# Optimization experiments

Measured on AMD Instinct MI355X. Metric: run time of the kernel, lower is better.

## Reference

```python
import jax, jax.numpy as jnp
import numpy as np


def setup_inputs() -> dict:
    key = jax.random.key(0)
    k1, k2, k3 = jax.random.split(key, 3)
    N, L, S, H, D = 2, 2048, 2048, 8, 64
    return {
        "queries": jax.random.normal(k1, (N, L, H, D), dtype=jnp.float32),
        "keys": jax.random.normal(k2, (N, S, H, D), dtype=jnp.float32),
        "values": jax.random.normal(k3, (N, S, H, D), dtype=jnp.float32),
        "q_mask": jnp.ones((N, L), dtype=bool),
        "kv_mask": jnp.ones((N, S), dtype=bool),
    }


def reference(queries, keys, values, q_mask, kv_mask):
    # QK^T: [N, L, S, H]
    qk = jnp.einsum("nlhd,nshd->nlsh", queries, keys)
    # mask: True where attention is allowed
    mask = q_mask[:, :, None, None] & kv_mask[:, None, :, None]
    qk = jnp.where(mask, qk, -jnp.inf)
    softmax_temp = 1.0 / np.sqrt(queries.shape[3]).astype(np.float32)
    A = jax.nn.softmax(softmax_temp * qk, axis=2)  # over S
    out = jnp.einsum("nlsh,nshd->nlhd", A, values)
    return out
```

## Files before the change

### kernel.cpp

```cpp
#include <hip/hip_runtime.h>
#include <hip/hip_bf16.h>

#define N_B 2
#define L_Q 2048
#define S_K 2048
#define N_H 8
#define D_H 64
#define HD  512
#define KVB 64
#define NT  32
#define RS  72
#define PQT ((size_t)N_B * L_Q * N_H)
#define LOG2E 1.4426950408889634f

typedef __attribute__((ext_vector_type(8))) short bf16x8;
typedef __attribute__((ext_vector_type(4))) short short4v;
typedef __attribute__((ext_vector_type(4))) float f32x4;

__device__ __forceinline__ short f2bf(float f) {
  union { float f; unsigned u; } v; v.f = f;
  return (short)((v.u + 0x7FFFu + ((v.u >> 16) & 1u)) >> 16);
}
__device__ __forceinline__ float bf2f(short s) {
  union { unsigned u; float f; } w; w.u = ((unsigned)(unsigned short)s) << 16;
  return w.f;
}
__device__ __forceinline__ bf16x8 pack8(float4 a, float4 b) {
  bf16x8 t;
  t[0]=f2bf(a.x); t[1]=f2bf(a.y); t[2]=f2bf(a.z); t[3]=f2bf(a.w);
  t[4]=f2bf(b.x); t[5]=f2bf(b.y); t[6]=f2bf(b.z); t[7]=f2bf(b.w);
  return t;
}

__global__ __launch_bounds__(256)
void preconv_kernel(const float* __restrict__ K, const float* __restrict__ V,
                    const int* __restrict__ kvm,
                    short* __restrict__ kws, short* __restrict__ vws,
                    unsigned long long* __restrict__ mws) {
  const size_t i = (size_t)blockIdx.x * 256 + threadIdx.x;
  const float4* kp = (const float4*)K + i * 2;
  float4 a = kp[0], b = kp[1];
  *(bf16x8*)(kws + i * 8) = pack8(a, b);
  const float4* vp = (const float4*)V + i * 2;
  float4 c = vp[0], d = vp[1];
  *(bf16x8*)(vws + i * 8) = pack8(c, d);
  if (blockIdx.x == 0 && threadIdx.x < (N_B * S_K / 64)) {
    const int* src = kvm + threadIdx.x * 64;
    unsigned long long m = 0;
    #pragma unroll 8
    for (int bb = 0; bb < 64; ++bb) m |= (src[bb] ? 1ull : 0ull) << bb;
    mws[threadIdx.x] = m;
  }
}

__global__ __launch_bounds__(256, 3)
void attn_fwd_v3(const float* __restrict__ Q, const short* __restrict__ Kb,
                 const short* __restrict__ Vb,
                 const unsigned long long* __restrict__ mbits,
                 float* __restrict__ Out,
                 float* __restrict__ Ow, float* __restrict__ Mw,
                 float* __restrict__ Lw, int split) {
  __shared__ __align__(128) short kt[2 * 4096];
  __shared__ __align__(128) short vt[2 * 4096];
  __shared__ __align__(16)  short pl[4][16 * RS];

  const int tid  = threadIdx.x;
  const int wid  = tid >> 6;
  const int lane = tid & 63;
  const int l16  = lane & 15;
  const int lg   = lane >> 4;

  const int per_xcd = gridDim.x >> 3;
  const int logical = (blockIdx.x & 7) * per_xcd + (blockIdx.x >> 3);
  int nh, sp, qb;
  if (split == 2) { nh = logical >> 6; sp = (logical >> 5) & 1; qb = logical & 31; }
  else            { nh = logical >> 5; sp = 0;                  qb = logical & 31; }
  const int n  = nh >> 3;
  const int h  = nh & 7;
  const int q0 = qb * 64 + wid * 16;
  const int tps = (split == 2) ? (NT / 2) : NT;
  const int t0 = sp * tps, t1 = t0 + tps;

  const float* Qn = Q + ((size_t)n * L_Q) * HD + h * D_H;
  const char*  Kn = (const char*)(Kb + ((size_t)n * S_K) * HD + h * D_H);
  const char*  Vn = (const char*)(Vb + ((size_t)n * S_K) * HD + h * D_H);

  int koffb[2], voffb[2];
  #pragma unroll
  for (int i = 0; i < 2; ++i) {
    const int p   = (wid * 2 + i) * 1024 + lane * 16;
    const int row = p >> 7;
    const int cb  = (p & 127) ^ ((row & 7) << 4);
    koffb[i] = row * 1024 + cb;
    const int k  = ((p >> 9) << 2) | ((p >> 5) & 3);
    const int d  = (((p >> 7) & 3) << 4) | ((p >> 1) & 15);
    voffb[i] = k * 1024 + d * 2;
  }

  bf16x8 qf[2];
  {
    const float* qp = Qn + (size_t)(q0 + l16) * HD + lg * 8;
    #pragma unroll
    for (int c = 0; c < 2; ++c) {
      float4 a = *(const float4*)(qp + c * 32);
      float4 b = *(const float4*)(qp + c * 32 + 4);
      float4 as, bs;
      as.x=a.x*0.125f; as.y=a.y*0.125f; as.z=a.z*0.125f; as.w=a.w*0.125f;
      bs.x=b.x*0.125f; bs.y=b.y*0.125f; bs.z=b.z*0.125f; bs.w=b.w*0.125f;
      qf[c] = pack8(as, bs);
    }
  }

  const int swz    = (l16 & 7) << 4;
  const int kaddrA = l16 * 128 + ((lg * 16) ^ swz);
  const int kaddrB = l16 * 128 + ((64 + lg * 16) ^ swz);
  const int vlane  = lg * 1024 + l16 * 8;
  const unsigned vt0 = (unsigned)(size_t)(__attribute__((address_space(3))) char*)((char*)&vt[0]);

  f32x4 o[4];
  #pragma unroll
  for (int g = 0; g < 4; ++g) o[g] = (f32x4){0.f, 0.f, 0.f, 0.f};
  float m_run[4], l_run[4];
  #pragma unroll
  for (int r = 0; r < 4; ++r) { m_run[r] = -3e38f; l_run[r] = 0.f; }

  short* pw = pl[wid];

  #define ISSUE(t_) do {                                                          \
    const int bs_ = ((t_) & 1) * 8192;                                            \
    const char* ks_ = Kn + (size_t)(t_) * 65536;                                  \
    const char* vs_ = Vn + (size_t)(t_) * 65536;                                  \
    _Pragma("unroll")                                                             \
    for (int i_ = 0; i_ < 2; ++i_) {                                              \
      __builtin_amdgcn_global_load_lds(                                           \
        (const __attribute__((address_space(1))) void*)(ks_ + koffb[i_]),         \
        (__attribute__((address_space(3))) void*)((char*)kt + bs_ + (wid*2+i_)*1024), \
        16, 0, 0);                                                                \
      __builtin_amdgcn_global_load_lds(                                           \
        (const __attribute__((address_space(1))) void*)(vs_ + voffb[i_]),         \
        (__attribute__((address_space(3))) void*)((char*)vt + bs_ + (wid*2+i_)*1024), \
        16, 0, 0);                                                                \
    }                                                                             \
  } while (0)

  ISSUE(t0);

  for (int t = t0; t < t1; ++t) {
    __syncthreads();
    if (t + 1 < t1) ISSUE(t + 1);
    const int bo = (t & 1) * 8192;

    f32x4 sc[4];
    #pragma unroll
    for (int g = 0; g < 4; ++g) {
      bf16x8 kb0 = *(const bf16x8*)((const char*)kt + bo + g * 2048 + kaddrA);
      bf16x8 kb1 = *(const bf16x8*)((const char*)kt + bo + g * 2048 + kaddrB);
      f32x4 z = (f32x4){0.f, 0.f, 0.f, 0.f};
      z = __builtin_amdgcn_mfma_f32_16x16x32_bf16(qf[0], kb0, z, 0, 0, 0);
      z = __builtin_amdgcn_mfma_f32_16x16x32_bf16(qf[1], kb1, z, 0, 0, 0);
      sc[g] = z;
    }

    const unsigned long long mb = mbits[n * NT + t];
    #pragma unroll
    for (int g = 0; g < 4; ++g) {
      if (!((mb >> (g * 16 + l16)) & 1ull)) {
        #pragma unroll
        for (int r = 0; r < 4; ++r) sc[g][r] = -3e38f;
      }
    }

    float mt[4];
    #pragma unroll
    for (int r = 0; r < 4; ++r) {
      float v = fmaxf(fmaxf(sc[0][r], sc[1][r]), fmaxf(sc[2][r], sc[3][r]));
      v = fmaxf(v, __shfl_xor(v, 1));
      v = fmaxf(v, __shfl_xor(v, 2));
      v = fmaxf(v, __shfl_xor(v, 4));
      v = fmaxf(v, __shfl_xor(v, 8));
      mt[r] = v;
    }
    float alpha[4];
    #pragma unroll
    for (int r = 0; r < 4; ++r) {
      float mn = fmaxf(m_run[r], mt[r]);
      alpha[r] = __builtin_amdgcn_exp2f((m_run[r] - mn) * LOG2E);
      m_run[r] = mn;
    }
    float rsum[4] = {0.f, 0.f, 0.f, 0.f};
    short pb[4][4];
    #pragma unroll
    for (int g = 0; g < 4; ++g) {
      #pragma unroll
      for (int r = 0; r < 4; ++r) {
        float p = __builtin_amdgcn_exp2f((sc[g][r] - m_run[r]) * LOG2E);
        short s = f2bf(p);
        pb[g][r] = s;
        rsum[r] += bf2f(s);
      }
    }
    #pragma unroll
    for (int r = 0; r < 4; ++r) {
      float v = rsum[r];
      v += __shfl_xor(v, 1);
      v += __shfl_xor(v, 2);
      v += __shfl_xor(v, 4);
      v += __shfl_xor(v, 8);
      l_run[r] = l_run[r] * alpha[r] + v;
    }
    #pragma unroll
    for (int g = 0; g < 4; ++g) {
      f32x4 tv = o[g];
      #pragma unroll
      for (int r = 0; r < 4; ++r) tv[r] *= alpha[r];
      o[g] = tv;
    }

    #pragma unroll
    for (int g = 0; g < 4; ++g)
      #pragma unroll
      for (int r = 0; r < 4; ++r)
        pw[(lg * 4 + r) * RS + g * 16 + l16] = pb[g][r];

    bf16x8 pa0 = *(const bf16x8*)&pw[l16 * RS + lg * 8];
    bf16x8 pa1 = *(const bf16x8*)&pw[l16 * RS + 32 + lg * 8];

    const unsigned va = vt0 + (unsigned)(bo + vlane);
    #define TRRD(dst, off) asm volatile("ds_read_b64_tr_b16 %0, %1 offset:" off \
                                        : "=v"(dst) : "v"(va))
    short4v w0la, w0lb, w0ha, w0hb, w1la, w1lb, w1ha, w1hb;
    short4v w2la, w2lb, w2ha, w2hb, w3la, w3lb, w3ha, w3hb;
    TRRD(w0la, "0");   TRRD(w0lb, "512"); TRRD(w0ha, "4096"); TRRD(w0hb, "4608");
    TRRD(w1la, "128"); TRRD(w1lb, "640"); TRRD(w1ha, "4224"); TRRD(w1hb, "4736");
    TRRD(w2la, "256"); TRRD(w2lb, "768"); TRRD(w2ha, "4352"); TRRD(w2hb, "4864");
    TRRD(w3la, "384"); TRRD(w3lb, "896"); TRRD(w3ha, "4480"); TRRD(w3hb, "4992");
    asm volatile("s_waitcnt lgkmcnt(0)" ::: "memory");
    __builtin_amdgcn_sched_barrier(0);

    bf16x8 v0l = __builtin_shufflevector(w0la, w0lb, 0,1,2,3,4,5,6,7);
    bf16x8 v0h = __builtin_shufflevector(w0ha, w0hb, 0,1,2,3,4,5,6,7);
    bf16x8 v1l = __builtin_shufflevector(w1la, w1lb, 0,1,2,3,4,5,6,7);
    bf16x8 v1h = __builtin_shufflevector(w1ha, w1hb, 0,1,2,3,4,5,6,7);
    bf16x8 v2l = __builtin_shufflevector(w2la, w2lb, 0,1,2,3,4,5,6,7);
    bf16x8 v2h = __builtin_shufflevector(w2ha, w2hb, 0,1,2,3,4,5,6,7);
    bf16x8 v3l = __builtin_shufflevector(w3la, w3lb, 0,1,2,3,4,5,6,7);
    bf16x8 v3h = __builtin_shufflevector(w3ha, w3hb, 0,1,2,3,4,5,6,7);

    o[0] = __builtin_amdgcn_mfma_f32_16x16x32_bf16(pa0, v0l, o[0], 0, 0, 0);
    o[0] = __builtin_amdgcn_mfma_f32_16x16x32_bf16(pa1, v0h, o[0], 0, 0, 0);
    o[1] = __builtin_amdgcn_mfma_f32_16x16x32_bf16(pa0, v1l, o[1], 0, 0, 0);
    o[1] = __builtin_amdgcn_mfma_f32_16x16x32_bf16(pa1, v1h, o[1], 0, 0, 0);
    o[2] = __builtin_amdgcn_mfma_f32_16x16x32_bf16(pa0, v2l, o[2], 0, 0, 0);
    o[2] = __builtin_amdgcn_mfma_f32_16x16x32_bf16(pa1, v2h, o[2], 0, 0, 0);
    o[3] = __builtin_amdgcn_mfma_f32_16x16x32_bf16(pa0, v3l, o[3], 0, 0, 0);
    o[3] = __builtin_amdgcn_mfma_f32_16x16x32_bf16(pa1, v3h, o[3], 0, 0, 0);
  }

  if (split == 2) {
    #pragma unroll
    for (int r = 0; r < 4; ++r) {
      const size_t row = ((size_t)n * L_Q + q0 + lg * 4 + r) * N_H + h;
      const size_t ob  = ((size_t)sp * PQT + row) * D_H;
      #pragma unroll
      for (int gd = 0; gd < 4; ++gd)
        Ow[ob + gd * 16 + l16] = o[gd][r];
      if (l16 == 0) { Mw[sp * PQT + row] = m_run[r]; Lw[sp * PQT + row] = l_run[r]; }
    }
  } else {
    float* op = Out + ((size_t)n * L_Q + q0) * HD + h * D_H;
    float inv[4];
    #pragma unroll
    for (int r = 0; r < 4; ++r) inv[r] = 1.0f / l_run[r];
    #pragma unroll
    for (int gd = 0; gd < 4; ++gd)
      #pragma unroll
      for (int r = 0; r < 4; ++r)
        op[(size_t)(lg * 4 + r) * HD + gd * 16 + l16] = o[gd][r] * inv[r];
  }
}

__global__ __launch_bounds__(256)
void combine_kernel(const float* __restrict__ Ow, const float* __restrict__ Mw,
                    const float* __restrict__ Lw, float* __restrict__ Out) {
  const int gid = blockIdx.x * 256 + threadIdx.x;
  const size_t rid = (size_t)(gid >> 4);
  const int d0 = (gid & 15) << 2;
  float m0 = Mw[rid],       l0 = Lw[rid];
  float m1 = Mw[PQT + rid], l1 = Lw[PQT + rid];
  float M  = fmaxf(m0, m1);
  float w0 = __builtin_amdgcn_exp2f((m0 - M) * LOG2E);
  float w1 = __builtin_amdgcn_exp2f((m1 - M) * LOG2E);
  float inv = 1.0f / (l0 * w0 + l1 * w1);
  const float4 o0 = *(const float4*)(Ow + rid * D_H + d0);
  const float4 o1 = *(const float4*)(Ow + (PQT + rid) * D_H + d0);
  float4 r;
  r.x = (o0.x * w0 + o1.x * w1) * inv;
  r.y = (o0.y * w0 + o1.y * w1) * inv;
  r.z = (o0.z * w0 + o1.z * w1) * inv;
  r.w = (o0.w * w0 + o1.w * w1) * inv;
  *(float4*)(Out + rid * D_H + d0) = r;
}

__global__ __launch_bounds__(256, 2)
void attn_fwd_kernel(const float* __restrict__ Q, const float* __restrict__ K,
                     const float* __restrict__ V,
                     const int* __restrict__ q_mask,
                     const int* __restrict__ kv_mask,
                     float* __restrict__ Out) {
  __shared__ __align__(16) short kts[KVB * RS];
  __shared__ __align__(16) short vts[D_H * RS];
  __shared__ __align__(16) short pls[4][16 * RS];
  const int tid = threadIdx.x, wid = tid >> 6, lane = tid & 63;
  const int l16 = lane & 15, lg = lane >> 4;
  const int bid = blockIdx.x, nh = bid >> 5, qb = bid & 31;
  const int n = nh >> 3, h = nh & 7, q0 = qb * 64 + wid * 16;
  const float* Qb = Q + ((size_t)n * L_Q) * HD + h * D_H;
  const float* Kb = K + ((size_t)n * S_K) * HD + h * D_H;
  const float* Vb = V + ((size_t)n * S_K) * HD + h * D_H;
  const int* km = kv_mask + (size_t)n * S_K;
  (void)q_mask;
  bf16x8 qf[2];
  {
    const float* qp = Qb + (size_t)(q0 + l16) * HD + lg * 8;
    #pragma unroll
    for (int c = 0; c < 2; ++c) {
      float4 a = *(const float4*)(qp + c * 32);
      float4 b = *(const float4*)(qp + c * 32 + 4);
      float4 as, bs;
      as.x=a.x*0.125f; as.y=a.y*0.125f; as.z=a.z*0.125f; as.w=a.w*0.125f;
      bs.x=b.x*0.125f; bs.y=b.y*0.125f; bs.z=b.z*0.125f; bs.w=b.w*0.125f;
      qf[c] = pack8(as, bs);
    }
  }
  f32x4 o[4];
  #pragma unroll
  for (int g = 0; g < 4; ++g) o[g] = (f32x4){0.f, 0.f, 0.f, 0.f};
  float m_run[4], l_run[4];
  #pragma unroll
  for (int r = 0; r < 4; ++r) { m_run[r] = -3e38f; l_run[r] = 0.f; }
  for (int s0 = 0; s0 < S_K; s0 += KVB) {
    __syncthreads();
    {
      const int cid = tid << 1, row = cid >> 3, c0 = cid & 7;
      const float* kp = Kb + (size_t)(s0 + row) * HD + c0 * 8;
      float4 f0 = *(const float4*)(kp), f1 = *(const float4*)(kp + 4);
      float4 f2 = *(const float4*)(kp + 8), f3 = *(const float4*)(kp + 12);
      *(bf16x8*)&kts[row * RS + c0 * 8]     = pack8(f0, f1);
      *(bf16x8*)&kts[row * RS + c0 * 8 + 8] = pack8(f2, f3);
    }
    {
      const int kv = tid >> 2, dc = tid & 3;
      const float* vp = Vb + (size_t)(s0 + kv) * HD + dc * 16;
      float4 f0 = *(const float4*)(vp), f1 = *(const float4*)(vp + 4);
      float4 f2 = *(const float4*)(vp + 8), f3 = *(const float4*)(vp + 12);
      float tv[16] = { f0.x,f0.y,f0.z,f0.w, f1.x,f1.y,f1.z,f1.w,
                       f2.x,f2.y,f2.z,f2.w, f3.x,f3.y,f3.z,f3.w };
      short* dst = &vts[(dc * 16) * RS + kv];
      #pragma unroll
      for (int j = 0; j < 16; ++j) dst[j * RS] = f2bf(tv[j]);
    }
    __syncthreads();
    f32x4 sc[4];
    #pragma unroll
    for (int g = 0; g < 4; ++g) {
      bf16x8 kb0 = *(const bf16x8*)&kts[(g*16 + l16) * RS + lg * 8];
      bf16x8 kb1 = *(const bf16x8*)&kts[(g*16 + l16) * RS + 32 + lg * 8];
      f32x4 z = (f32x4){0.f, 0.f, 0.f, 0.f};
      z = __builtin_amdgcn_mfma_f32_16x16x32_bf16(qf[0], kb0, z, 0, 0, 0);
      z = __builtin_amdgcn_mfma_f32_16x16x32_bf16(qf[1], kb1, z, 0, 0, 0);
      sc[g] = z;
    }
    #pragma unroll
    for (int g = 0; g < 4; ++g) {
      float b = km[s0 + g*16 + l16] ? 0.f : -3e38f;
      #pragma unroll
      for (int r = 0; r < 4; ++r) sc[g][r] += b;
    }
    float mt[4];
    #pragma unroll
    for (int r = 0; r < 4; ++r) {
      float v = fmaxf(fmaxf(sc[0][r], sc[1][r]), fmaxf(sc[2][r], sc[3][r]));
      v = fmaxf(v, __shfl_xor(v, 1)); v = fmaxf(v, __shfl_xor(v, 2));
      v = fmaxf(v, __shfl_xor(v, 4)); v = fmaxf(v, __shfl_xor(v, 8));
      mt[r] = v;
    }
    float alpha[4];
    #pragma unroll
    for (int r = 0; r < 4; ++r) {
      float mn = fmaxf(m_run[r], mt[r]);
      alpha[r] = __builtin_amdgcn_exp2f((m_run[r] - mn) * LOG2E);
      m_run[r] = mn;
    }
    float rsum[4] = {0.f, 0.f, 0.f, 0.f};
    short pb[4][4];
    #pragma unroll
    for (int g = 0; g < 4; ++g)
      #pragma unroll
      for (int r = 0; r < 4; ++r) {
        float p = __builtin_amdgcn_exp2f((sc[g][r] - m_run[r]) * LOG2E);
        short s = f2bf(p); pb[g][r] = s; rsum[r] += bf2f(s);
      }
    #pragma unroll
    for (int r = 0; r < 4; ++r) {
      float v = rsum[r];
      v += __shfl_xor(v, 1); v += __shfl_xor(v, 2);
      v += __shfl_xor(v, 4); v += __shfl_xor(v, 8);
      l_run[r] = l_run[r] * alpha[r] + v;
    }
    #pragma unroll
    for (int g = 0; g < 4; ++g)
      #pragma unroll
      for (int r = 0; r < 4; ++r) o[g][r] *= alpha[r];
    short* pwf = pls[wid];
    #pragma unroll
    for (int g = 0; g < 4; ++g)
      #pragma unroll
      for (int r = 0; r < 4; ++r)
        pwf[(lg*4 + r) * RS + g*16 + l16] = pb[g][r];
    __syncthreads();
    bf16x8 pa0 = *(const bf16x8*)&pwf[l16 * RS + lg * 8];
    bf16x8 pa1 = *(const bf16x8*)&pwf[l16 * RS + 32 + lg * 8];
    #pragma unroll
    for (int gd = 0; gd < 4; ++gd) {
      bf16x8 vb0 = *(const bf16x8*)&vts[(gd*16 + l16) * RS + lg * 8];
      bf16x8 vb1 = *(const bf16x8*)&vts[(gd*16 + l16) * RS + 32 + lg * 8];
      o[gd] = __builtin_amdgcn_mfma_f32_16x16x32_bf16(pa0, vb0, o[gd], 0, 0, 0);
      o[gd] = __builtin_amdgcn_mfma_f32_16x16x32_bf16(pa1, vb1, o[gd], 0, 0, 0);
    }
  }
  float* op = Out + ((size_t)n * L_Q + q0) * HD + h * D_H;
  float inv[4];
  #pragma unroll
  for (int r = 0; r < 4; ++r) inv[r] = 1.0f / l_run[r];
  #pragma unroll
  for (int gd = 0; gd < 4; ++gd)
    #pragma unroll
    for (int r = 0; r < 4; ++r)
      op[(size_t)(lg*4 + r) * HD + gd*16 + l16] = o[gd][r] * inv[r];
}

extern "C" void kernel_launch(void* const* d_in, const int* in_sizes, int n_in,
                              void* d_out, int out_size, void* d_ws, size_t ws_size,
                              hipStream_t stream) {
  const float* Q = (const float*)d_in[0];
  const float* K = (const float*)d_in[1];
  const float* V = (const float*)d_in[2];
  const int* qm = (const int*)d_in[3];
  const int* km = (const int*)d_in[4];
  float* Out = (float*)d_out;
  (void)in_sizes; (void)n_in; (void)out_size;

  const size_t kbytes  = (size_t)N_B * S_K * HD * 2;
  const size_t need1   = 2 * kbytes + 1024;
  const size_t owbytes = 2 * PQT * D_H * sizeof(float);
  const size_t mlbytes = 2 * PQT * sizeof(float);
  const size_t need2   = need1 + owbytes + 2 * mlbytes;

  if (ws_size >= need1) {
    short* kws = (short*)d_ws;
    short* vws = (short*)((char*)d_ws + kbytes);
    unsigned long long* mws = (unsigned long long*)((char*)d_ws + 2 * kbytes);
    hipLaunchKernelGGL(preconv_kernel, dim3(1024), dim3(256), 0, stream,
                       K, V, km, kws, vws, mws);
    if (ws_size >= need2) {
      float* Ow = (float*)((char*)d_ws + need1);
      float* Mw = (float*)((char*)d_ws + need1 + owbytes);
      float* Lw = (float*)((char*)d_ws + need1 + owbytes + mlbytes);
      hipLaunchKernelGGL(attn_fwd_v3, dim3(1024), dim3(256), 0, stream,
                         Q, kws, vws, mws, Out, Ow, Mw, Lw, 2);
      hipLaunchKernelGGL(combine_kernel, dim3(2048), dim3(256), 0, stream,
                         Ow, Mw, Lw, Out);
    } else {
      hipLaunchKernelGGL(attn_fwd_v3, dim3(512), dim3(256), 0, stream,
                         Q, kws, vws, mws, Out, (float*)d_ws, (float*)d_ws,
                         (float*)d_ws, 1);
    }
  } else {
    hipLaunchKernelGGL(attn_fwd_kernel, dim3(512), dim3(256), 0, stream,
                       Q, K, V, qm, km, Out);
  }
}
```

Before: 148.1 us.

## Defer softmax rescaling, MFMA row sums, fold log2e into Q, 4-way KV split

Folds log2(e) into the Q pre-scale so the exponentials become bare exp2 calls. Replaces the per-tile cross-lane max and rescale with a lazy update that runs only when a new score exceeds the running max by a threshold. Row sums are now computed with an MFMA against a ones vector instead of shuffle reductions. The KV split is generalised so the attention kernel can run with 4 splits when workspace allows, with a combine kernel that merges any number of splits. This trims VALU and shuffle work in the inner loop and adds parallelism, at the cost of extra partial-output traffic and a heavier combine step, and it relies on the threshold keeping unnormalised exponentials within float range.

```diff
diff --git a/kernel.cpp b/kernel.cpp
--- a/kernel.cpp
+++ b/kernel.cpp
@@ -12,6 +12,7 @@
 #define RS  72
 #define PQT ((size_t)N_B * L_Q * N_H)
 #define LOG2E 1.4426950408889634f
+#define DEFER_THR 11.5f
 
 typedef __attribute__((ext_vector_type(8))) short bf16x8;
 typedef __attribute__((ext_vector_type(4))) short short4v;
@@ -54,12 +55,12 @@
 }
 
 __global__ __launch_bounds__(256, 3)
-void attn_fwd_v3(const float* __restrict__ Q, const short* __restrict__ Kb,
+void attn_fwd_v4(const float* __restrict__ Q, const short* __restrict__ Kb,
                  const short* __restrict__ Vb,
                  const unsigned long long* __restrict__ mbits,
                  float* __restrict__ Out,
                  float* __restrict__ Ow, float* __restrict__ Mw,
-                 float* __restrict__ Lw, int split) {
+                 float* __restrict__ Lw, int spbits) {
   __shared__ __align__(128) short kt[2 * 4096];
   __shared__ __align__(128) short vt[2 * 4096];
   __shared__ __align__(16)  short pl[4][16 * RS];
@@ -72,13 +73,14 @@
 
   const int per_xcd = gridDim.x >> 3;
   const int logical = (blockIdx.x & 7) * per_xcd + (blockIdx.x >> 3);
-  int nh, sp, qb;
-  if (split == 2) { nh = logical >> 6; sp = (logical >> 5) & 1; qb = logical & 31; }
-  else            { nh = logical >> 5; sp = 0;                  qb = logical & 31; }
+  const int qb   = logical & 31;
+  const int rest = logical >> 5;
+  const int sp   = rest & ((1 << spbits) - 1);
+  const int nh   = rest >> spbits;
   const int n  = nh >> 3;
   const int h  = nh & 7;
   const int q0 = qb * 64 + wid * 16;
-  const int tps = (split == 2) ? (NT / 2) : NT;
+  const int tps = NT >> spbits;
   const int t0 = sp * tps, t1 = t0 + tps;
 
   const float* Qn = Q + ((size_t)n * L_Q) * HD + h * D_H;
@@ -99,17 +101,22 @@
 
   bf16x8 qf[2];
   {
+    const float sc_q = 0.125f * LOG2E;
     const float* qp = Qn + (size_t)(q0 + l16) * HD + lg * 8;
     #pragma unroll
     for (int c = 0; c < 2; ++c) {
       float4 a = *(const float4*)(qp + c * 32);
       float4 b = *(const float4*)(qp + c * 32 + 4);
       float4 as, bs;
-      as.x=a.x*0.125f; as.y=a.y*0.125f; as.z=a.z*0.125f; as.w=a.w*0.125f;
-      bs.x=b.x*0.125f; bs.y=b.y*0.125f; bs.z=b.z*0.125f; bs.w=b.w*0.125f;
+      as.x=a.x*sc_q; as.y=a.y*sc_q; as.z=a.z*sc_q; as.w=a.w*sc_q;
+      bs.x=b.x*sc_q; bs.y=b.y*sc_q; bs.z=b.z*sc_q; bs.w=b.w*sc_q;
       qf[c] = pack8(as, bs);
     }
   }
+
+  bf16x8 onesf;
+  #pragma unroll
+  for (int i = 0; i < 8; ++i) onesf[i] = (short)0x3F80;
 
   const int swz    = (l16 & 7) << 4;
   const int kaddrA = l16 * 128 + ((lg * 16) ^ swz);
@@ -120,9 +127,10 @@
   f32x4 o[4];
   #pragma unroll
   for (int g = 0; g < 4; ++g) o[g] = (f32x4){0.f, 0.f, 0.f, 0.f};
-  float m_run[4], l_run[4];
-  #pragma unroll
-  for (int r = 0; r < 4; ++r) { m_run[r] = -3e38f; l_run[r] = 0.f; }
+  f32x4 ls = (f32x4){0.f, 0.f, 0.f, 0.f};
+  float m_run[4];
+  #pragma unroll
+  for (int r = 0; r < 4; ++r) m_run[r] = 0.f;
 
   short* pw = pl[wid];
 
@@ -170,51 +178,39 @@
       }
     }
 
-    float mt[4];
-    #pragma unroll
-    for (int r = 0; r < 4; ++r) {
-      float v = fmaxf(fmaxf(sc[0][r], sc[1][r]), fmaxf(sc[2][r], sc[3][r]));
-      v = fmaxf(v, __shfl_xor(v, 1));
-      v = fmaxf(v, __shfl_xor(v, 2));
-      v = fmaxf(v, __shfl_xor(v, 4));
-      v = fmaxf(v, __shfl_xor(v, 8));
-      mt[r] = v;
-    }
-    float alpha[4];
-    #pragma unroll
-    for (int r = 0; r < 4; ++r) {
-      float mn = fmaxf(m_run[r], mt[r]);
-      alpha[r] = __builtin_amdgcn_exp2f((m_run[r] - mn) * LOG2E);
-      m_run[r] = mn;
-    }
-    float rsum[4] = {0.f, 0.f, 0.f, 0.f};
+    float pr[4];
+    #pragma unroll
+    for (int r = 0; r < 4; ++r)
+      pr[r] = fmaxf(fmaxf(sc[0][r], sc[1][r]), fmaxf(sc[2][r], sc[3][r]));
+    bool ok = (pr[0] <= m_run[0] + DEFER_THR) & (pr[1] <= m_run[1] + DEFER_THR) &
+              (pr[2] <= m_run[2] + DEFER_THR) & (pr[3] <= m_run[3] + DEFER_THR);
+    if (!__all(ok)) {
+      float alpha[4];
+      #pragma unroll
+      for (int r = 0; r < 4; ++r) {
+        float v = pr[r];
+        v = fmaxf(v, __shfl_xor(v, 1));
+        v = fmaxf(v, __shfl_xor(v, 2));
+        v = fmaxf(v, __shfl_xor(v, 4));
+        v = fmaxf(v, __shfl_xor(v, 8));
+        float mn = fmaxf(m_run[r], v);
+        alpha[r] = __builtin_amdgcn_exp2f(m_run[r] - mn);
+        m_run[r] = mn;
+      }
+      #pragma unroll
+      for (int g = 0; g < 4; ++g)
+        #pragma unroll
+        for (int r = 0; r < 4; ++r) o[g][r] *= alpha[r];
+      #pragma unroll
+      for (int r = 0; r < 4; ++r) ls[r] *= alpha[r];
+    }
+
     short pb[4][4];
     #pragma unroll
-    for (int g = 0; g < 4; ++g) {
-      #pragma unroll
-      for (int r = 0; r < 4; ++r) {
-        float p = __builtin_amdgcn_exp2f((sc[g][r] - m_run[r]) * LOG2E);
-        short s = f2bf(p);
-        pb[g][r] = s;
-        rsum[r] += bf2f(s);
-      }
-    }
-    #pragma unroll
-    for (int r = 0; r < 4; ++r) {
-      float v = rsum[r];
-      v += __shfl_xor(v, 1);
-      v += __shfl_xor(v, 2);
-      v += __shfl_xor(v, 4);
-      v += __shfl_xor(v, 8);
-      l_run[r] = l_run[r] * alpha[r] + v;
-    }
-    #pragma unroll
-    for (int g = 0; g < 4; ++g) {
-      f32x4 tv = o[g];
-      #pragma unroll
-      for (int r = 0; r < 4; ++r) tv[r] *= alpha[r];
-      o[g] = tv;
-    }
+    for (int g = 0; g < 4; ++g)
+      #pragma unroll
+      for (int r = 0; r < 4; ++r)
+        pb[g][r] = f2bf(__builtin_amdgcn_exp2f(sc[g][r] - m_run[r]));
 
     #pragma unroll
     for (int g = 0; g < 4; ++g)
@@ -224,6 +220,9 @@
 
     bf16x8 pa0 = *(const bf16x8*)&pw[l16 * RS + lg * 8];
     bf16x8 pa1 = *(const bf16x8*)&pw[l16 * RS + 32 + lg * 8];
+
+    ls = __builtin_amdgcn_mfma_f32_16x16x32_bf16(pa0, onesf, ls, 0, 0, 0);
+    ls = __builtin_amdgcn_mfma_f32_16x16x32_bf16(pa1, onesf, ls, 0, 0, 0);
 
     const unsigned va = vt0 + (unsigned)(bo + vlane);
     #define TRRD(dst, off) asm volatile("ds_read_b64_tr_b16 %0, %1 offset:" off \
@@ -256,7 +255,7 @@
     o[3] = __builtin_amdgcn_mfma_f32_16x16x32_bf16(pa1, v3h, o[3], 0, 0, 0);
   }
 
-  if (split == 2) {
+  if (spbits > 0) {
     #pragma unroll
     for (int r = 0; r < 4; ++r) {
       const size_t row = ((size_t)n * L_Q + q0 + lg * 4 + r) * N_H + h;
@@ -264,13 +263,13 @@
       #pragma unroll
       for (int gd = 0; gd < 4; ++gd)
         Ow[ob + gd * 16 + l16] = o[gd][r];
-      if (l16 == 0) { Mw[sp * PQT + row] = m_run[r]; Lw[sp * PQT + row] = l_run[r]; }
+      if (l16 == 0) { Mw[sp * PQT + row] = m_run[r]; Lw[sp * PQT + row] = ls[r]; }
     }
   } else {
     float* op = Out + ((size_t)n * L_Q + q0) * HD + h * D_H;
     float inv[4];
     #pragma unroll
-    for (int r = 0; r < 4; ++r) inv[r] = 1.0f / l_run[r];
+    for (int r = 0; r < 4; ++r) inv[r] = 1.0f / ls[r];
     #pragma unroll
     for (int gd = 0; gd < 4; ++gd)
       #pragma unroll
@@ -281,23 +280,24 @@
 
 __global__ __launch_bounds__(256)
 void combine_kernel(const float* __restrict__ Ow, const float* __restrict__ Mw,
-                    const float* __restrict__ Lw, float* __restrict__ Out) {
+                    const float* __restrict__ Lw, float* __restrict__ Out,
+                    int nsp) {
   const int gid = blockIdx.x * 256 + threadIdx.x;
   const size_t rid = (size_t)(gid >> 4);
   const int d0 = (gid & 15) << 2;
-  float m0 = Mw[rid],       l0 = Lw[rid];
-  float m1 = Mw[PQT + rid], l1 = Lw[PQT + rid];
-  float M  = fmaxf(m0, m1);
-  float w0 = __builtin_amdgcn_exp2f((m0 - M) * LOG2E);
-  float w1 = __builtin_amdgcn_exp2f((m1 - M) * LOG2E);
-  float inv = 1.0f / (l0 * w0 + l1 * w1);
-  const float4 o0 = *(const float4*)(Ow + rid * D_H + d0);
-  const float4 o1 = *(const float4*)(Ow + (PQT + rid) * D_H + d0);
+  float M = -3e38f;
+  for (int j = 0; j < nsp; ++j) M = fmaxf(M, Mw[j * PQT + rid]);
+  float lsum = 0.f;
+  float ax = 0.f, ay = 0.f, az = 0.f, aw = 0.f;
+  for (int j = 0; j < nsp; ++j) {
+    float w = __builtin_amdgcn_exp2f(Mw[j * PQT + rid] - M);
+    lsum += Lw[j * PQT + rid] * w;
+    const float4 ov = *(const float4*)(Ow + (j * PQT + rid) * D_H + d0);
+    ax += ov.x * w; ay += ov.y * w; az += ov.z * w; aw += ov.w * w;
+  }
+  const float inv = 1.0f / lsum;
   float4 r;
-  r.x = (o0.x * w0 + o1.x * w1) * inv;
-  r.y = (o0.y * w0 + o1.y * w1) * inv;
-  r.z = (o0.z * w0 + o1.z * w1) * inv;
-  r.w = (o0.w * w0 + o1.w * w1) * inv;
+  r.x = ax * inv; r.y = ay * inv; r.z = az * inv; r.w = aw * inv;
   *(float4*)(Out + rid * D_H + d0) = r;
 }
 
@@ -450,11 +450,10 @@
   float* Out = (float*)d_out;
   (void)in_sizes; (void)n_in; (void)out_size;
 
-  const size_t kbytes  = (size_t)N_B * S_K * HD * 2;
-  const size_t need1   = 2 * kbytes + 1024;
-  const size_t owbytes = 2 * PQT * D_H * sizeof(float);
-  const size_t mlbytes = 2 * PQT * sizeof(float);
-  const size_t need2   = need1 + owbytes + 2 * mlbytes;
+  const size_t kbytes = (size_t)N_B * S_K * HD * 2;
+  const size_t need1  = 2 * kbytes + 1024;
+  const size_t per_sp = PQT * D_H * sizeof(float)
+                      + 2 * PQT * sizeof(float);
 
   if (ws_size >= need1) {
     short* kws = (short*)d_ws;
@@ -462,18 +461,24 @@
     unsigned long long* mws = (unsigned long long*)((char*)d_ws + 2 * kbytes);
     hipLaunchKernelGGL(preconv_kernel, dim3(1024), dim3(256), 0, stream,
                        K, V, km, kws, vws, mws);
-    if (ws_size >= need2) {
-      float* Ow = (float*)((char*)d_ws + need1);
-      float* Mw = (float*)((char*)d_ws + need1 + owbytes);
-      float* Lw = (float*)((char*)d_ws + need1 + owbytes + mlbytes);
-      hipLaunchKernelGGL(attn_fwd_v3, dim3(1024), dim3(256), 0, stream,
-                         Q, kws, vws, mws, Out, Ow, Mw, Lw, 2);
+
+    int spbits = 0;
+    if (ws_size >= need1 + 4 * per_sp)      spbits = 2;
+    else if (ws_size >= need1 + 2 * per_sp) spbits = 1;
+
+    if (spbits > 0) {
+      const int nsp = 1 << spbits;
+      float* Mw = (float*)((char*)d_ws + need1);
+      float* Lw = Mw + (size_t)nsp * PQT;
+      float* Ow = Lw + (size_t)nsp * PQT;
+      hipLaunchKernelGGL(attn_fwd_v4, dim3(512 * nsp), dim3(256), 0, stream,
+                         Q, kws, vws, mws, Out, Ow, Mw, Lw, spbits);
       hipLaunchKernelGGL(combine_kernel, dim3(2048), dim3(256), 0, stream,
-                         Ow, Mw, Lw, Out);
+                         Ow, Mw, Lw, Out, nsp);
     } else {
-      hipLaunchKernelGGL(attn_fwd_v3, dim3(512), dim3(256), 0, stream,
+      hipLaunchKernelGGL(attn_fwd_v4, dim3(512), dim3(256), 0, stream,
                          Q, kws, vws, mws, Out, (float*)d_ws, (float*)d_ws,
-                         (float*)d_ws, 1);
+                         (float*)d_ws, 0);
     }
   } else {
     hipLaunchKernelGGL(attn_fwd_kernel, dim3(512), dim3(256), 0, stream,
```

New measurement: 125.2 us. 15.5% less time.
